# Optimization experiments

Hardware: AMD Instinct MI355X
Metric: run time of the kernel (lower is better)

## Reference

```python
import jax, jax.numpy as jnp
import numpy as np

Q, A, D = 8192, 2048, 64
SQ2 = 1.4142135623730951
SQ6 = 2.449489742783178
SQ2_3 = 0.816496580927726


def _y2_from_dir(d):
    # d: [..., 3] unit (or zero) directions -> degree-2 real SH coeffs [..., 5]
    x, y, z = d[..., 0], d[..., 1], d[..., 2]
    xx, yy, zz = x * x, y * y, z * z
    xy, xz, yz = x * y, x * z, y * z
    c0 = (xx - yy) / SQ2
    c1 = (-xx - yy + 2.0 * zz) / SQ6
    c2 = SQ2 * xy
    c3 = SQ2 * xz
    c4 = SQ2 * yz
    return jnp.stack([c0, c1, c2, c3, c4], axis=-1)


def _reconstruct_quadrupole(c):
    # c: [A, 5] -> symmetric traceless [A, 3, 3]
    c0, c1, c2, c3, c4 = c[..., 0], c[..., 1], c[..., 2], c[..., 3], c[..., 4]
    zz = c1 * SQ2_3
    xx = 0.5 * (c0 * SQ2 - zz)
    yy = 0.5 * (-c0 * SQ2 - zz)
    xy = c2 / SQ2
    xz = c3 / SQ2
    yz = c4 / SQ2
    return jnp.stack([xx, xy, xz, xy, yy, yz, xz, yz, zz], axis=-1).reshape(*c.shape[:-1], 3, 3)


def setup_inputs() -> dict:
    key = jax.random.key(0)
    ks = jax.random.split(key, 12)
    query_coords = jax.random.uniform(ks[0], (Q, 3), dtype=jnp.float32) * 10.0
    atom_coords = jax.random.uniform(ks[1], (A, 3), dtype=jnp.float32) * 10.0
    alpha = 0.3 + 0.7 * jax.random.uniform(ks[2], (A,), dtype=jnp.float32)
    even_scalar = jax.random.normal(ks[3], (A, D), dtype=jnp.float32) * 0.5
    odd_scalar = jax.random.normal(ks[4], (A, D), dtype=jnp.float32) * 0.5
    odd_vector = jax.random.normal(ks[5], (A, D, 3), dtype=jnp.float32) * 0.5
    even_vector = jax.random.normal(ks[6], (A, D, 3), dtype=jnp.float32) * 0.5
    even_tensor = jax.random.normal(ks[7], (A, D, 5), dtype=jnp.float32) * 0.5
    odd_tensor = jax.random.normal(ks[8], (A, D, 5), dtype=jnp.float32) * 0.5
    W_readout = jax.random.normal(ks[9], (10, D), dtype=jnp.float32) / np.sqrt(D)
    b_readout = jax.random.normal(ks[10], (10,), dtype=jnp.float32) * 0.01
    return {
        'query_coords': query_coords, 'atom_coords': atom_coords, 'alpha': alpha,
        'even_scalar': even_scalar, 'odd_scalar': odd_scalar,
        'odd_vector': odd_vector, 'even_vector': even_vector,
        'even_tensor': even_tensor, 'odd_tensor': odd_tensor,
        'W_readout': W_readout, 'b_readout': b_readout,
    }


def _forward(query_coords, atom_coords, alpha, even_scalar, odd_scalar,
             odd_vector, even_vector, even_tensor, odd_tensor, W_readout, b_readout):
    # readout weight order: e0, o0, vec_odd, vec_even, ten_even, ten_odd, a1o, a1e, a2e, a2o
    w_e0, w_o0, w_vo, w_ve, w_te, w_to, w_a1, w_a1e, w_a2, w_a2o = [W_readout[i] for i in range(10)]
    b_e0, b_o0, b_vo, b_ve, b_te, b_to, b_a1, b_a1e, b_a2, b_a2o = [b_readout[i] for i in range(10)]

    # Gaussian radial kernel with per-atom alpha
    rel = query_coords[:, None, :] - atom_coords[None, :, :]          # [Q, A, 3]
    dist2 = jnp.sum(rel * rel, axis=-1)                               # [Q, A]
    dist = jnp.sqrt(jnp.maximum(dist2, 1e-16))
    weights = jnp.exp(-alpha[None, :] * dist2)                        # [Q, A]
    weight_sum = jnp.maximum(jnp.sum(weights, axis=1, keepdims=True), 1e-8)
    nw = weights / weight_sum                                         # normalized_weights [Q, A]

    dist_c = jnp.maximum(dist, 1e-8)
    direction = jnp.where(dist[..., None] > 1e-6, rel / dist_c[..., None], 0.0)  # [Q, A, 3]
    y1 = direction                                                    # [Q, A, 3]
    y2 = _y2_from_dir(direction)                                      # [Q, A, 5]

    # per-atom scalar readouts
    c0e = even_scalar @ w_e0 + b_e0                                   # [A]
    c0o = odd_scalar @ w_o0 + b_o0                                    # [A]
    dipole_coeff = jnp.einsum('adi,d->ai', odd_vector, w_vo) + b_vo   # [A, 3]
    bivector_coeff = jnp.einsum('adi,d->ai', even_vector, w_ve) + b_ve
    quad_coeff = jnp.einsum('adk,d->ak', even_tensor, w_te) + b_te    # [A, 5]
    odd_quad_coeff = jnp.einsum('adk,d->ak', odd_tensor, w_to) + b_to

    quadrupole = _reconstruct_quadrupole(quad_coeff)                  # [A, 3, 3]
    odd_quadrupole = _reconstruct_quadrupole(odd_quad_coeff)
    quad_vector = jnp.einsum('aij,qaj->qai', quadrupole, direction)   # [Q, A, 3]
    odd_quad_vector = jnp.einsum('aij,qaj->qai', odd_quadrupole, direction)

    scalar_field = nw @ c0e                                           # [Q]
    pseudoscalar_field = nw @ c0o
    dipole_field = jnp.einsum('qa,ai->qi', nw, dipole_coeff)          # [Q, 3]
    quadrupole_field = jnp.sum(nw[..., None] * quad_vector, axis=1)
    vector_field = dipole_field + quadrupole_field
    bivector_seed = jnp.einsum('qa,ai->qi', nw, bivector_coeff)
    odd_quadrupole_field = jnp.sum(nw[..., None] * odd_quad_vector, axis=1)
    bivector_field = bivector_seed + odd_quadrupole_field

    # angular terms: contract (features . Y) over D with readout weight
    angular_1o = jnp.einsum('qai,adi,d->qa', y1, odd_vector, w_a1) + b_a1
    angular_1e = jnp.einsum('qai,adi,d->qa', y1, even_vector, w_a1e) + b_a1e
    angular_2e = jnp.einsum('qak,adk,d->qa', y2, even_tensor, w_a2) + b_a2
    angular_2o = jnp.einsum('qak,adk,d->qa', y2, odd_tensor, w_a2o) + b_a2o
    even_angular = jnp.sum(nw * (angular_1o + angular_2e), axis=1)    # [Q]
    odd_angular = jnp.sum(nw * (angular_1e + angular_2o), axis=1)

    multivector = jnp.zeros((query_coords.shape[0], 16), dtype=query_coords.dtype)
    multivector = multivector.at[:, 0].set(scalar_field)
    multivector = multivector.at[:, 1:4].set(vector_field)
    multivector = multivector.at[:, 5].set(bivector_field[:, 2])
    multivector = multivector.at[:, 6].set(-bivector_field[:, 1])
    multivector = multivector.at[:, 7].set(bivector_field[:, 0])
    multivector = multivector.at[:, 11].set(pseudoscalar_field)

    even_contrib = scalar_field + even_angular
    odd_contrib = pseudoscalar_field + odd_angular
    total = (even_contrib + odd_contrib
             + 0.1 * jnp.linalg.norm(vector_field, axis=-1)
             + 0.05 * jnp.linalg.norm(bivector_field, axis=-1))
    return total, even_contrib, odd_contrib, multivector


def reference(query_coords, atom_coords, alpha, even_scalar, odd_scalar,
              odd_vector, even_vector, even_tensor, odd_tensor, W_readout, b_readout):
    return _forward(query_coords, atom_coords, alpha, even_scalar, odd_scalar,
                    odd_vector, even_vector, even_tensor, odd_tensor, W_readout, b_readout)
```

## Files before the change

### kernel.cpp

```cpp
#include <hip/hip_runtime.h>
#include <math.h>

#define QN 8192
#define AN 2048
#define DN 64
#define NSPLIT 32
#define CHUNK 64
#define AH 136

#define SQ2f      1.4142135623730951f
#define INV_SQ2f  0.7071067811865476f
#define SQ6_INVf  0.4082482904638631f
#define SQ2_3f    0.816496580927726f
#define LOG2Ef    1.4426950408889634f

typedef __attribute__((ext_vector_type(8))) _Float16 half8;
typedef __attribute__((ext_vector_type(4))) float f32x4;

__device__ __forceinline__ float wave_sum(float v) {
#pragma unroll
  for (int off = 32; off > 0; off >>= 1) v += __shfl_xor(v, off, 64);
  return v;
}

__device__ __forceinline__ unsigned pkh(float a, float b) {
  auto h = __builtin_amdgcn_cvt_pkrtz(a, b);
  return __builtin_bit_cast(unsigned, h);
}

__global__ __launch_bounds__(256) void precompute_pack(
    const float* __restrict__ atom_coords, const float* __restrict__ alpha,
    const float* __restrict__ even_scalar, const float* __restrict__ odd_scalar,
    const float* __restrict__ odd_vector, const float* __restrict__ even_vector,
    const float* __restrict__ even_tensor, const float* __restrict__ odd_tensor,
    const float* __restrict__ W, const float* __restrict__ b,
    _Float16* __restrict__ Mh, float4* __restrict__ atomC)
{
  const int a = blockIdx.x * 4 + (threadIdx.x >> 6);
  const int d = threadIdx.x & 63;

  const float es  = even_scalar[a * DN + d];
  const float os  = odd_scalar[a * DN + d];
  const float ov0 = odd_vector[(a * DN + d) * 3 + 0];
  const float ov1 = odd_vector[(a * DN + d) * 3 + 1];
  const float ov2 = odd_vector[(a * DN + d) * 3 + 2];
  const float ev0 = even_vector[(a * DN + d) * 3 + 0];
  const float ev1 = even_vector[(a * DN + d) * 3 + 1];
  const float ev2 = even_vector[(a * DN + d) * 3 + 2];
  const float et0 = even_tensor[(a * DN + d) * 5 + 0];
  const float et1 = even_tensor[(a * DN + d) * 5 + 1];
  const float et2 = even_tensor[(a * DN + d) * 5 + 2];
  const float et3 = even_tensor[(a * DN + d) * 5 + 3];
  const float et4 = even_tensor[(a * DN + d) * 5 + 4];
  const float ot0 = odd_tensor[(a * DN + d) * 5 + 0];
  const float ot1 = odd_tensor[(a * DN + d) * 5 + 1];
  const float ot2 = odd_tensor[(a * DN + d) * 5 + 2];
  const float ot3 = odd_tensor[(a * DN + d) * 5 + 3];
  const float ot4 = odd_tensor[(a * DN + d) * 5 + 4];

  const float w0 = W[0 * DN + d];
  const float w1 = W[1 * DN + d];
  const float w2 = W[2 * DN + d];
  const float w3 = W[3 * DN + d];
  const float w4 = W[4 * DN + d];
  const float w5 = W[5 * DN + d];
  const float w6 = W[6 * DN + d];
  const float w7 = W[7 * DN + d];
  const float w8 = W[8 * DN + d];
  const float w9 = W[9 * DN + d];

  float r[34];
  r[0]  = es * w0;
  r[1]  = os * w1;
  r[2]  = ov0 * w2; r[3]  = ov1 * w2; r[4]  = ov2 * w2;
  r[5]  = ev0 * w3; r[6]  = ev1 * w3; r[7]  = ev2 * w3;
  r[8]  = et0 * w4; r[9]  = et1 * w4; r[10] = et2 * w4; r[11] = et3 * w4; r[12] = et4 * w4;
  r[13] = ot0 * w5; r[14] = ot1 * w5; r[15] = ot2 * w5; r[16] = ot3 * w5; r[17] = ot4 * w5;
  r[18] = ov0 * w6; r[19] = ov1 * w6; r[20] = ov2 * w6;
  r[21] = ev0 * w7; r[22] = ev1 * w7; r[23] = ev2 * w7;
  r[24] = et0 * w8; r[25] = et1 * w8; r[26] = et2 * w8; r[27] = et3 * w8; r[28] = et4 * w8;
  r[29] = ot0 * w9; r[30] = ot1 * w9; r[31] = ot2 * w9; r[32] = ot3 * w9; r[33] = ot4 * w9;

#pragma unroll
  for (int k = 0; k < 34; ++k) r[k] = wave_sum(r[k]);

  if (d < 16) {
    const float eb = b[4];
    const float ec0 = r[8] + eb, ec1 = r[9] + eb, ec2 = r[10] + eb,
                ec3 = r[11] + eb, ec4 = r[12] + eb;
    const float Qzz = ec1 * SQ2_3f;
    const float Qxx = 0.5f * (ec0 * SQ2f - Qzz);
    const float Qyy = 0.5f * (-ec0 * SQ2f - Qzz);
    const float Qxy = ec2 * INV_SQ2f, Qxz = ec3 * INV_SQ2f, Qyz = ec4 * INV_SQ2f;
    const float ob = b[5];
    const float oc0 = r[13] + ob, oc1 = r[14] + ob, oc2 = r[15] + ob,
                oc3 = r[16] + ob, oc4 = r[17] + ob;
    const float Ozz = oc1 * SQ2_3f;
    const float Oxx = 0.5f * (oc0 * SQ2f - Ozz);
    const float Oyy = 0.5f * (-oc0 * SQ2f - Ozz);
    const float Oxy = oc2 * INV_SQ2f, Oxz = oc3 * INV_SQ2f, Oyz = oc4 * INV_SQ2f;
    const float A0e = r[24] * INV_SQ2f, A1e = r[25] * SQ6_INVf;
    const float A2e = r[26] * SQ2f, A3e = r[27] * SQ2f, A4e = r[28] * SQ2f;
    const float qe_xx = A0e - A1e, qe_yy = -A0e - A1e, qe_zz = 2.0f * A1e;
    const float A0o = r[29] * INV_SQ2f, A1o = r[30] * SQ6_INVf;
    const float A2o = r[31] * SQ2f, A3o = r[32] * SQ2f, A4o = r[33] * SQ2f;
    const float qo_xx = A0o - A1o, qo_yy = -A0o - A1o, qo_zz = 2.0f * A1o;

    float m[8];
#pragma unroll
    for (int k = 0; k < 8; ++k) m[k] = 0.f;
    switch (d) {
      case 0:  m[0] = 1.f; break;
      case 1:  m[0] = r[0] + b[0]; break;
      case 2:  m[0] = r[1] + b[1]; break;
      case 3:  m[0]=r[2]+b[2]; m[1]=Qxx; m[2]=Qxy; m[3]=Qxz; break;
      case 4:  m[0]=r[3]+b[2]; m[1]=Qxy; m[2]=Qyy; m[3]=Qyz; break;
      case 5:  m[0]=r[4]+b[2]; m[1]=Qxz; m[2]=Qyz; m[3]=Qzz; break;
      case 6:  m[0]=r[5]+b[3]; m[1]=Oxx; m[2]=Oxy; m[3]=Oxz; break;
      case 7:  m[0]=r[6]+b[3]; m[1]=Oxy; m[2]=Oyy; m[3]=Oyz; break;
      case 8:  m[0]=r[7]+b[3]; m[1]=Oxz; m[2]=Oyz; m[3]=Ozz; break;
      case 9:  m[0]=qe_zz; m[1]=r[18]; m[2]=r[19]; m[3]=r[20]; break;
      case 10: m[0]=qo_zz; m[1]=r[21]; m[2]=r[22]; m[3]=r[23]; break;
      case 12: m[0]=qe_xx-qe_zz; m[1]=qe_yy-qe_zz;
               m[2]=A2e; m[3]=A3e; m[4]=A4e; break;
      case 13: m[0]=qo_xx-qo_zz; m[1]=qo_yy-qo_zz;
               m[2]=A2o; m[3]=A3o; m[4]=A4o; break;
      default: break;
    }
    union { unsigned u[4]; half8 h; } row;
    row.u[0] = pkh(m[0], m[1]);
    row.u[1] = pkh(m[2], m[3]);
    row.u[2] = pkh(m[4], m[5]);
    row.u[3] = pkh(m[6], m[7]);
    *(half8*)(Mh + (size_t)a * AH + d * 8) = row.h;
  } else if (d == 16) {
    atomC[a] = make_float4(atom_coords[a * 3 + 0], atom_coords[a * 3 + 1],
                           atom_coords[a * 3 + 2], -alpha[a] * LOG2Ef);
  }
}

__global__ __launch_bounds__(256, 4) void mfma_splat(
    const float* __restrict__ qcoord, const _Float16* __restrict__ Mh,
    const float4* __restrict__ atomC, float* __restrict__ P)
{
  __shared__ __align__(16) _Float16 smM[CHUNK * AH];
  __shared__ float4 smC[CHUNK];
  const int tid = threadIdx.x;
  const int abase = blockIdx.y * CHUNK;

  {
    const float4* src = (const float4*)(Mh + (size_t)abase * AH);
    float4* dst = (float4*)smM;
#pragma unroll
    for (int t = 0; t < 4; ++t) dst[tid + t * 256] = src[tid + t * 256];
    if (tid < 64) dst[1024 + tid] = src[1024 + tid];
  }
  if (tid < CHUNK) smC[tid] = atomC[abase + tid];

  const int lane = tid & 63;
  const int wid = tid >> 6;
  const int fq = lane & 15;
  const int g = (lane >> 4) & 3;
  const int qb = blockIdx.x * 256 + wid * 64;

  float qx[4], qy[4], qz[4];
#pragma unroll
  for (int jt = 0; jt < 4; ++jt) {
    const int q = qb + jt * 16 + fq;
    qx[jt] = qcoord[q * 3 + 0];
    qy[jt] = qcoord[q * 3 + 1];
    qz[jt] = qcoord[q * 3 + 2];
  }

  const int a1off = (fq < 11 ? fq : 11) * 8;
  const int a2off = 96 + (fq == 9 ? 0 : (fq == 10 ? 8 : 16));
  const _Float16* p1 = smM + g * AH + a1off;
  const _Float16* p2 = smM + g * AH + a2off;

  __syncthreads();

  f32x4 acc[4];
#pragma unroll
  for (int jt = 0; jt < 4; ++jt) acc[jt] = (f32x4){0.f, 0.f, 0.f, 0.f};

  for (int it = 0; it < CHUNK / 4; ++it) {
    const half8 a1 = *(const half8*)(p1 + it * (4 * AH));
    const half8 a2 = *(const half8*)(p2 + it * (4 * AH));
    const float4 ca = smC[it * 4 + g];

#pragma unroll
    for (int jt = 0; jt < 4; ++jt) {
      const float dx = qx[jt] - ca.x, dy = qy[jt] - ca.y, dz = qz[jt] - ca.z;
      const float d2 = fmaf(dx, dx, fmaf(dy, dy, dz * dz));
      const float w = __builtin_amdgcn_exp2f(ca.w * d2);
      const float inv = __builtin_amdgcn_rsqf(d2);
      const float g1 = w * inv;
      const float g2 = g1 * inv;
      const float m1 = g1 * dx, m2 = g1 * dy, m3 = g1 * dz;
      const float t = g2 * dx, u = g2 * dy;
      const float m4 = t * dx, m6 = t * dy, m7 = t * dz;
      const float m5 = u * dy, m8 = u * dz;

      union { unsigned uu[4]; half8 h; } b1, b2;
      b1.uu[0] = pkh(w, m1);   b1.uu[1] = pkh(m2, m3);
      b1.uu[2] = 0u;           b1.uu[3] = 0u;
      b2.uu[0] = pkh(m4, m5);  b2.uu[1] = pkh(m6, m7);
      b2.uu[2] = pkh(m8, 0.f); b2.uu[3] = 0u;

      acc[jt] = __builtin_amdgcn_mfma_f32_16x16x32_f16(a1, b1.h, acc[jt], 0, 0, 0);
      acc[jt] = __builtin_amdgcn_mfma_f32_16x16x32_f16(a2, b2.h, acc[jt], 0, 0, 0);
    }
  }

  const int frow = (lane >> 4) * 4;
#pragma unroll
  for (int jt = 0; jt < 4; ++jt) {
    float* Pb = P + (size_t)blockIdx.y * 16 * QN + qb + jt * 16 + fq;
#pragma unroll
    for (int r = 0; r < 4; ++r) {
      const int f = frow + r;
      if (f < 11) Pb[(size_t)f * QN] = acc[jt][r];
    }
  }
}

__global__ __launch_bounds__(256) void reduce_combine(
    const float* __restrict__ P, const float* __restrict__ b,
    float* __restrict__ out)
{
  __shared__ float sm[11][8][32];
  const int tid = threadIdx.x;
  const int ql = tid & 31;
  const int sg = tid >> 5;
  const int q = blockIdx.x * 32 + ql;

  float acc[11];
#pragma unroll
  for (int f = 0; f < 11; ++f) acc[f] = 0.f;
#pragma unroll
  for (int j = 0; j < 4; ++j) {
    const int s = sg * 4 + j;
    const float* Ps = P + (size_t)s * 16 * QN + q;
#pragma unroll
    for (int f = 0; f < 11; ++f) acc[f] += Ps[(size_t)f * QN];
  }
#pragma unroll
  for (int f = 0; f < 11; ++f) sm[f][sg][ql] = acc[f];
  __syncthreads();

  if (tid < 32) {
    float a[11];
#pragma unroll
    for (int f = 0; f < 11; ++f) {
      float v = 0.f;
#pragma unroll
      for (int s = 0; s < 8; ++s) v += sm[f][s][tid];
      a[f] = v;
    }
    const int qq = blockIdx.x * 32 + tid;
    const float b_ea = b[6] + b[8];
    const float b_oa = b[7] + b[9];

    const float Sw = fmaxf(a[0], 1e-8f);
    const float inv = 1.0f / Sw;
    const float snw = a[0] * inv;
    const float scal = a[1] * inv;
    const float pse  = a[2] * inv;
    const float vx = a[3] * inv;
    const float vy = a[4] * inv;
    const float vz = a[5] * inv;
    const float bx = a[6] * inv;
    const float by = a[7] * inv;
    const float bz = a[8] * inv;
    const float ea = fmaf(b_ea, snw, a[9] * inv);
    const float oa = fmaf(b_oa, snw, a[10] * inv);

    const float evenc = scal + ea;
    const float oddc  = pse + oa;
    const float vn = sqrtf(fmaf(vx, vx, fmaf(vy, vy, vz * vz)));
    const float bn = sqrtf(fmaf(bx, bx, fmaf(by, by, bz * bz)));
    const float total = evenc + oddc + 0.1f * vn + 0.05f * bn;

    out[qq] = total;
    out[QN + qq] = evenc;
    out[2 * QN + qq] = oddc;
    float* mv = out + 3 * QN + (size_t)qq * 16;
    mv[0] = scal;
    mv[1] = vx; mv[2] = vy; mv[3] = vz;
    mv[4] = 0.f;
    mv[5] = bz; mv[6] = -by; mv[7] = bx;
    mv[8] = 0.f; mv[9] = 0.f; mv[10] = 0.f;
    mv[11] = pse;
    mv[12] = 0.f; mv[13] = 0.f; mv[14] = 0.f; mv[15] = 0.f;
  }
}

extern "C" void kernel_launch(void* const* d_in, const int* in_sizes, int n_in,
                              void* d_out, int out_size, void* d_ws, size_t ws_size,
                              hipStream_t stream) {
  const float* query_coords = (const float*)d_in[0];
  const float* atom_coords  = (const float*)d_in[1];
  const float* alpha        = (const float*)d_in[2];
  const float* even_scalar  = (const float*)d_in[3];
  const float* odd_scalar   = (const float*)d_in[4];
  const float* odd_vector   = (const float*)d_in[5];
  const float* even_vector  = (const float*)d_in[6];
  const float* even_tensor  = (const float*)d_in[7];
  const float* odd_tensor   = (const float*)d_in[8];
  const float* W            = (const float*)d_in[9];
  const float* b            = (const float*)d_in[10];
  float* out = (float*)d_out;

  const size_t mhBytes = (size_t)AN * AH * sizeof(_Float16);
  char* ws = (char*)d_ws;
  _Float16*  Mh     = (_Float16*)ws;
  float4*    atomCp = (float4*)(ws + mhBytes);
  float*     P      = (float*)(ws + mhBytes + (size_t)AN * sizeof(float4));

  precompute_pack<<<AN / 4, 256, 0, stream>>>(
      atom_coords, alpha, even_scalar, odd_scalar, odd_vector, even_vector,
      even_tensor, odd_tensor, W, b, Mh, atomCp);
  mfma_splat<<<dim3(QN / 256, NSPLIT), 256, 0, stream>>>(
      query_coords, Mh, atomCp, P);
  reduce_combine<<<QN / 32, 256, 0, stream>>>(P, b, out);
}
```

Before: 36.88 us.

## Replace split-partial buffer and reduce pass with global atomic accumulation

The splat kernel now atomically adds its per-split feature sums into an 11×Q accumulator. The old code wrote a 32-way partial buffer that a separate reduction kernel then read back. The accumulator is zeroed inside the precompute kernel, and the final kernel becomes a simple per-query finalize. The per-wave query tile also shrinks from 4 to 2 MFMA tiles, which doubles the grid, and the occupancy hint rises to 6. This removes the partial-buffer round trip and the shared-memory reduction. In exchange it adds contention on float atomics, makes summation order nondeterministic, and means each atom chunk is staged into LDS by twice as many blocks.

```diff
diff --git a/kernel.cpp b/kernel.cpp
--- a/kernel.cpp
+++ b/kernel.cpp
@@ -7,6 +7,7 @@
 #define NSPLIT 32
 #define CHUNK 64
 #define AH 136
+#define NQ 2
 
 #define SQ2f      1.4142135623730951f
 #define INV_SQ2f  0.7071067811865476f
@@ -34,8 +35,14 @@
     const float* __restrict__ odd_vector, const float* __restrict__ even_vector,
     const float* __restrict__ even_tensor, const float* __restrict__ odd_tensor,
     const float* __restrict__ W, const float* __restrict__ b,
-    _Float16* __restrict__ Mh, float4* __restrict__ atomC)
+    _Float16* __restrict__ Mh, float4* __restrict__ atomC,
+    float* __restrict__ Acc)
 {
+  {
+    const int zi = blockIdx.x * 256 + threadIdx.x;
+    if (zi < 11 * QN) Acc[zi] = 0.f;
+  }
+
   const int a = blockIdx.x * 4 + (threadIdx.x >> 6);
   const int d = threadIdx.x & 63;
 
@@ -139,9 +146,9 @@
   }
 }
 
-__global__ __launch_bounds__(256, 4) void mfma_splat(
+__global__ __launch_bounds__(256, 6) void mfma_splat(
     const float* __restrict__ qcoord, const _Float16* __restrict__ Mh,
-    const float4* __restrict__ atomC, float* __restrict__ P)
+    const float4* __restrict__ atomC, float* __restrict__ Acc)
 {
   __shared__ __align__(16) _Float16 smM[CHUNK * AH];
   __shared__ float4 smC[CHUNK];
@@ -161,11 +168,11 @@
   const int wid = tid >> 6;
   const int fq = lane & 15;
   const int g = (lane >> 4) & 3;
-  const int qb = blockIdx.x * 256 + wid * 64;
-
-  float qx[4], qy[4], qz[4];
-#pragma unroll
-  for (int jt = 0; jt < 4; ++jt) {
+  const int qb = blockIdx.x * 128 + wid * 32;
+
+  float qx[NQ], qy[NQ], qz[NQ];
+#pragma unroll
+  for (int jt = 0; jt < NQ; ++jt) {
     const int q = qb + jt * 16 + fq;
     qx[jt] = qcoord[q * 3 + 0];
     qy[jt] = qcoord[q * 3 + 1];
@@ -179,9 +186,9 @@
 
   __syncthreads();
 
-  f32x4 acc[4];
-#pragma unroll
-  for (int jt = 0; jt < 4; ++jt) acc[jt] = (f32x4){0.f, 0.f, 0.f, 0.f};
+  f32x4 acc[NQ];
+#pragma unroll
+  for (int jt = 0; jt < NQ; ++jt) acc[jt] = (f32x4){0.f, 0.f, 0.f, 0.f};
 
   for (int it = 0; it < CHUNK / 4; ++it) {
     const half8 a1 = *(const half8*)(p1 + it * (4 * AH));
@@ -189,7 +196,7 @@
     const float4 ca = smC[it * 4 + g];
 
 #pragma unroll
-    for (int jt = 0; jt < 4; ++jt) {
+    for (int jt = 0; jt < NQ; ++jt) {
       const float dx = qx[jt] - ca.x, dy = qy[jt] - ca.y, dz = qz[jt] - ca.z;
       const float d2 = fmaf(dx, dx, fmaf(dy, dy, dz * dz));
       const float w = __builtin_amdgcn_exp2f(ca.w * d2);
@@ -214,85 +221,59 @@
 
   const int frow = (lane >> 4) * 4;
 #pragma unroll
-  for (int jt = 0; jt < 4; ++jt) {
-    float* Pb = P + (size_t)blockIdx.y * 16 * QN + qb + jt * 16 + fq;
+  for (int jt = 0; jt < NQ; ++jt) {
+    const int q = qb + jt * 16 + fq;
 #pragma unroll
     for (int r = 0; r < 4; ++r) {
       const int f = frow + r;
-      if (f < 11) Pb[(size_t)f * QN] = acc[jt][r];
+      if (f < 11) atomicAdd(&Acc[(size_t)f * QN + q], acc[jt][r]);
     }
   }
 }
 
-__global__ __launch_bounds__(256) void reduce_combine(
-    const float* __restrict__ P, const float* __restrict__ b,
+__global__ __launch_bounds__(256) void finalize(
+    const float* __restrict__ Acc, const float* __restrict__ b,
     float* __restrict__ out)
 {
-  __shared__ float sm[11][8][32];
-  const int tid = threadIdx.x;
-  const int ql = tid & 31;
-  const int sg = tid >> 5;
-  const int q = blockIdx.x * 32 + ql;
-
-  float acc[11];
-#pragma unroll
-  for (int f = 0; f < 11; ++f) acc[f] = 0.f;
-#pragma unroll
-  for (int j = 0; j < 4; ++j) {
-    const int s = sg * 4 + j;
-    const float* Ps = P + (size_t)s * 16 * QN + q;
-#pragma unroll
-    for (int f = 0; f < 11; ++f) acc[f] += Ps[(size_t)f * QN];
-  }
-#pragma unroll
-  for (int f = 0; f < 11; ++f) sm[f][sg][ql] = acc[f];
-  __syncthreads();
-
-  if (tid < 32) {
-    float a[11];
-#pragma unroll
-    for (int f = 0; f < 11; ++f) {
-      float v = 0.f;
-#pragma unroll
-      for (int s = 0; s < 8; ++s) v += sm[f][s][tid];
-      a[f] = v;
-    }
-    const int qq = blockIdx.x * 32 + tid;
-    const float b_ea = b[6] + b[8];
-    const float b_oa = b[7] + b[9];
-
-    const float Sw = fmaxf(a[0], 1e-8f);
-    const float inv = 1.0f / Sw;
-    const float snw = a[0] * inv;
-    const float scal = a[1] * inv;
-    const float pse  = a[2] * inv;
-    const float vx = a[3] * inv;
-    const float vy = a[4] * inv;
-    const float vz = a[5] * inv;
-    const float bx = a[6] * inv;
-    const float by = a[7] * inv;
-    const float bz = a[8] * inv;
-    const float ea = fmaf(b_ea, snw, a[9] * inv);
-    const float oa = fmaf(b_oa, snw, a[10] * inv);
-
-    const float evenc = scal + ea;
-    const float oddc  = pse + oa;
-    const float vn = sqrtf(fmaf(vx, vx, fmaf(vy, vy, vz * vz)));
-    const float bn = sqrtf(fmaf(bx, bx, fmaf(by, by, bz * bz)));
-    const float total = evenc + oddc + 0.1f * vn + 0.05f * bn;
-
-    out[qq] = total;
-    out[QN + qq] = evenc;
-    out[2 * QN + qq] = oddc;
-    float* mv = out + 3 * QN + (size_t)qq * 16;
-    mv[0] = scal;
-    mv[1] = vx; mv[2] = vy; mv[3] = vz;
-    mv[4] = 0.f;
-    mv[5] = bz; mv[6] = -by; mv[7] = bx;
-    mv[8] = 0.f; mv[9] = 0.f; mv[10] = 0.f;
-    mv[11] = pse;
-    mv[12] = 0.f; mv[13] = 0.f; mv[14] = 0.f; mv[15] = 0.f;
-  }
+  const int q = blockIdx.x * 256 + threadIdx.x;
+  float a[11];
+#pragma unroll
+  for (int f = 0; f < 11; ++f) a[f] = Acc[(size_t)f * QN + q];
+
+  const float b_ea = b[6] + b[8];
+  const float b_oa = b[7] + b[9];
+
+  const float Sw = fmaxf(a[0], 1e-8f);
+  const float inv = 1.0f / Sw;
+  const float snw = a[0] * inv;
+  const float scal = a[1] * inv;
+  const float pse  = a[2] * inv;
+  const float vx = a[3] * inv;
+  const float vy = a[4] * inv;
+  const float vz = a[5] * inv;
+  const float bx = a[6] * inv;
+  const float by = a[7] * inv;
+  const float bz = a[8] * inv;
+  const float ea = fmaf(b_ea, snw, a[9] * inv);
+  const float oa = fmaf(b_oa, snw, a[10] * inv);
+
+  const float evenc = scal + ea;
+  const float oddc  = pse + oa;
+  const float vn = sqrtf(fmaf(vx, vx, fmaf(vy, vy, vz * vz)));
+  const float bn = sqrtf(fmaf(bx, bx, fmaf(by, by, bz * bz)));
+  const float total = evenc + oddc + 0.1f * vn + 0.05f * bn;
+
+  out[q] = total;
+  out[QN + q] = evenc;
+  out[2 * QN + q] = oddc;
+  float* mv = out + 3 * QN + (size_t)q * 16;
+  mv[0] = scal;
+  mv[1] = vx; mv[2] = vy; mv[3] = vz;
+  mv[4] = 0.f;
+  mv[5] = bz; mv[6] = -by; mv[7] = bx;
+  mv[8] = 0.f; mv[9] = 0.f; mv[10] = 0.f;
+  mv[11] = pse;
+  mv[12] = 0.f; mv[13] = 0.f; mv[14] = 0.f; mv[15] = 0.f;
 }
 
 extern "C" void kernel_launch(void* const* d_in, const int* in_sizes, int n_in,
@@ -315,12 +296,12 @@
   char* ws = (char*)d_ws;
   _Float16*  Mh     = (_Float16*)ws;
   float4*    atomCp = (float4*)(ws + mhBytes);
-  float*     P      = (float*)(ws + mhBytes + (size_t)AN * sizeof(float4));
+  float*     Acc    = (float*)(ws + mhBytes + (size_t)AN * sizeof(float4));
 
   precompute_pack<<<AN / 4, 256, 0, stream>>>(
       atom_coords, alpha, even_scalar, odd_scalar, odd_vector, even_vector,
-      even_tensor, odd_tensor, W, b, Mh, atomCp);
-  mfma_splat<<<dim3(QN / 256, NSPLIT), 256, 0, stream>>>(
-      query_coords, Mh, atomCp, P);
-  reduce_combine<<<QN / 32, 256, 0, stream>>>(P, b, out);
-}
+      even_tensor, odd_tensor, W, b, Mh, atomCp, Acc);
+  mfma_splat<<<dim3(QN / 128, NSPLIT), 256, 0, stream>>>(
+      query_coords, Mh, atomCp, Acc);
+  finalize<<<QN / 256, 256, 0, stream>>>(Acc, b, out);
+}
```

After: 30.79 us. 1.2x faster.
